# Performance work log

Hardware: AMD Instinct MI355X
Metric: run time of the kernel (lower is better)

Reference implementation:

```python
import jax, jax.numpy as jnp
import numpy as np

B, N, D = 64, 784, 768
H, HD, G = 32, 24, 2
HID = 3072
SCALE = HD ** -0.5
EPS = 1e-6


def _ln(x, g, b):
    m = jnp.mean(x, -1, keepdims=True)
    v = jnp.mean((x - m) ** 2, -1, keepdims=True)
    return (x - m) * jax.lax.rsqrt(v + EPS) * g + b


def setup_inputs() -> dict:
    key = jax.random.key(0)
    ks = jax.random.split(key, 12)
    def rn(k, shape, s=0.02):
        return (jax.random.normal(k, shape) * s).astype(jnp.float32)
    return {
        'x_cls': jax.random.normal(ks[0], (B, 1, D), jnp.float32),
        'x_img': jax.random.normal(ks[1], (B, N, D), jnp.float32),
        'ln1_g': jnp.ones((D,), jnp.float32), 'ln1_b': jnp.zeros((D,), jnp.float32),
        'Wq': rn(ks[2], (D, D)), 'bq': jnp.zeros((D,), jnp.float32),
        'Wk': rn(ks[3], (D, D)), 'bk': jnp.zeros((D,), jnp.float32),
        'Wv': rn(ks[4], (D, D)), 'bv': jnp.zeros((D,), jnp.float32),
        'w1_W': rn(ks[5], (H, H), 0.1), 'w1_b': jnp.zeros((H,), jnp.float32),
        'w2_W': rn(ks[6], (H, H), 0.1), 'w2_b': jnp.zeros((H,), jnp.float32),
        'proj_W': rn(ks[7], (D, D)), 'proj_b': jnp.zeros((D,), jnp.float32),
        'ln2_g': jnp.ones((D,), jnp.float32), 'ln2_b': jnp.zeros((D,), jnp.float32),
        'fc1_W': rn(ks[8], (G, HID // G, D // G)), 'fc1_b': jnp.zeros((G, HID // G), jnp.float32),
        'fc2_W': rn(ks[9], (G, D // G, HID // G)), 'fc2_b': jnp.zeros((G, D // G), jnp.float32),
    }


def reference(x_cls, x_img, ln1_g, ln1_b, Wq, bq, Wk, bk, Wv, bv,
              w1_W, w1_b, w2_W, w2_b, proj_W, proj_b, ln2_g, ln2_b,
              fc1_W, fc1_b, fc2_W, fc2_b):
    # --- ClassAttention (non-mismatch path), dropout = identity (eval) ---
    u = jnp.concatenate([x_cls, x_img], axis=1)  # [B, M, D], M = N+1
    M = u.shape[1]
    n = _ln(u, ln1_g, ln1_b)
    q = ((n[:, :1] @ Wq + bq).reshape(B, 1, H, HD).transpose(0, 2, 1, 3)) * SCALE  # [B,H,1,HD]
    k = (n @ Wk + bk).reshape(B, M, H, HD).transpose(0, 2, 1, 3)                   # [B,H,M,HD]
    v = (n @ Wv + bv).reshape(B, M, H, HD).transpose(0, 2, 1, 3)
    attn = jnp.einsum('bhqd,bhkd->bhqk', q, k)  # [B,H,1,M]
    # interactive score mixing across heads (w1 pre-softmax, w2 post-softmax)
    attn = attn + jnp.einsum('bhqk,hg->bgqk', attn, w1_W) + w1_b[None, :, None, None]
    attn = jax.nn.softmax(attn, axis=-1)
    attn = attn + jnp.einsum('bhqk,hg->bgqk', attn, w2_W) + w2_b[None, :, None, None]
    o = jnp.einsum('bhqk,bhkd->bhqd', attn, v).transpose(0, 2, 1, 3).reshape(B, 1, D)
    x_cls = x_cls + (o @ proj_W + proj_b)
    # --- GroupConvMlp on the cls token (grouped 1x1 convs + channel shuffle) ---
    y = _ln(x_cls, ln2_g, ln2_b)
    h = jnp.einsum('btgc,goc->btgo', y.reshape(B, 1, G, D // G), fc1_W) + fc1_b  # group-major out channels
    h = jax.nn.gelu(h.reshape(B, 1, HID), approximate=False)
    # channel_shuffle(group=G): out channel b*gc+a = in channel a*G+b
    h = h.reshape(B, 1, HID // G, G).transpose(0, 1, 3, 2).reshape(B, 1, HID)
    z = jnp.einsum('btgc,goc->btgo', h.reshape(B, 1, G, HID // G), fc2_W) + fc2_b
    x_cls = x_cls + z.reshape(B, 1, D)
    return (x_cls, x_img)
```

## Files before the change

### kernel.cpp

```cpp
#include <hip/hip_runtime.h>
#include <hip/hip_bf16.h>
#include <math.h>

#define BB   64
#define NN   784
#define DD   768
#define HH   32
#define HD24 24
#define MM   785
#define HIDN 3072
#define QSCALE 0.20412414523193154f
#define LNEPS 1e-6f

#define WS_Q     0
#define WS_RS    49152
#define WS_RM    100352
#define WS_S1P   151552
#define WS_BQP   163840
#define WS_LMX   176128
#define WS_LSM   184320
#define WS_A2P   192512
#define WS_WMP   200704
#define WS_PS    208896
#define WS_C1    210432
#define WS_H2    259584
#define WS_O     456192
#define WS_E     505344
#define WS_T     2143744
#define WS_ZP    0

typedef __attribute__((ext_vector_type(8))) short bf16x8;
typedef __attribute__((ext_vector_type(4))) float f32x4;

__device__ __forceinline__ unsigned packbf(float a, float b) {
  union { __hip_bfloat162 h2; unsigned u; } cv;
  cv.h2 = __float22bfloat162_rn(make_float2(a, b));
  return cv.u;
}

__global__ __launch_bounds__(256) void k_q(
    const float* __restrict__ x_cls,
    const float* __restrict__ g1, const float* __restrict__ b1,
    const float* __restrict__ Wq, const float* __restrict__ bq,
    float* __restrict__ ws)
{
  const int b = blockIdx.y;
  const int oc0 = blockIdx.x * 64;
  const int t = threadIdx.x;
  const int lane = t & 63, wid = t >> 6;

  __shared__ __align__(16) float nc_l[DD];
  __shared__ float red4[4][64];
  __shared__ float rS[4], rQ[4];
  __shared__ float musd[2];

  float xv[3];
  float s = 0.f, q2 = 0.f;
#pragma unroll
  for (int k = 0; k < 3; ++k) {
    float v = x_cls[(size_t)b * DD + t + 256 * k];
    xv[k] = v; s += v; q2 += v * v;
  }
#pragma unroll
  for (int off = 1; off < 64; off <<= 1) { s += __shfl_xor(s, off); q2 += __shfl_xor(q2, off); }
  if (lane == 0) { rS[wid] = s; rQ[wid] = q2; }
  __syncthreads();
  if (t == 0) {
    float ss = rS[0] + rS[1] + rS[2] + rS[3];
    float qq = rQ[0] + rQ[1] + rQ[2] + rQ[3];
    float mu = ss * (1.f / DD);
    musd[0] = mu; musd[1] = rsqrtf(qq * (1.f / DD) - mu * mu + LNEPS);
  }
  __syncthreads();
  {
    float mu = musd[0], rs = musd[1];
#pragma unroll
    for (int k = 0; k < 3; ++k) {
      int d = t + 256 * k;
      nc_l[d] = (xv[k] - mu) * rs * g1[d] + b1[d];
    }
  }
  __syncthreads();

  const int oc = t & 63, ks = t >> 6;
  const float* wp = Wq + (size_t)(ks * 192) * DD + oc0 + oc;
  const float* ncp = nc_l + ks * 192;
  float a0 = 0.f, a1 = 0.f, a2 = 0.f, a3 = 0.f;
#pragma unroll 4
  for (int d = 0; d < 192; d += 4) {
    a0 += ncp[d + 0] * wp[(size_t)(d + 0) * DD];
    a1 += ncp[d + 1] * wp[(size_t)(d + 1) * DD];
    a2 += ncp[d + 2] * wp[(size_t)(d + 2) * DD];
    a3 += ncp[d + 3] * wp[(size_t)(d + 3) * DD];
  }
  red4[ks][oc] = (a0 + a1) + (a2 + a3);
  __syncthreads();
  if (t < 64) {
    int ocg = oc0 + t;
    ws[WS_Q + (size_t)b * DD + ocg] =
        (red4[0][t] + red4[1][t] + red4[2][t] + red4[3][t] + bq[ocg]) * QSCALE;
  }
}

__global__ __launch_bounds__(256) void k_gqk(
    const float* __restrict__ g1, const float* __restrict__ b1,
    const float* __restrict__ Wk, const float* __restrict__ w1W,
    float* __restrict__ ws)
{
  const int b = blockIdx.y;
  const int d0 = blockIdx.x * 128;
  const int t = threadIdx.x;

  __shared__ __align__(16) float q_l[DD];
  __shared__ float T1[HH * HH];
  __shared__ float qk_l[128][33];
  __shared__ float pS[8][HH], pB[8][HH];

  for (int i = t; i < DD; i += 256) q_l[i] = ws[WS_Q + (size_t)b * DD + i];
  for (int i = t; i < HH * HH; i += 256) {
    int g = i >> 5, h = i & 31;
    T1[i] = w1W[i] + ((g == h) ? 1.f : 0.f);
  }
  __syncthreads();

  {
    const int dl = t >> 1, gh = t & 1;
    const float4* wr = (const float4*)(Wk + (size_t)(d0 + dl) * DD + gh * 384);
    const float4* qr = (const float4*)(q_l + gh * 384);
#pragma unroll 4
    for (int gg = 0; gg < 16; ++gg) {
      float a = 0.f;
#pragma unroll
      for (int c = 0; c < 6; ++c) {
        float4 w = wr[gg * 6 + c];
        float4 p = qr[gg * 6 + c];
        a += w.x * p.x + w.y * p.y + w.z * p.z + w.w * p.w;
      }
      qk_l[dl][gh * 16 + gg] = a;
    }
  }
  __syncthreads();
  {
    const int h = t & 31, dg = t >> 5;
    float fb[16];
    float s1a = 0.f, bqa = 0.f;
#pragma unroll 2
    for (int dd = 0; dd < 16; ++dd) {
      int dl = dg * 16 + dd;
      float f = 0.f;
#pragma unroll 8
      for (int g = 0; g < HH; ++g) f += qk_l[dl][g] * T1[g * HH + h];
      float gq = g1[d0 + dl] * f;
      fb[dd] = gq;
      s1a += gq;
      bqa += b1[d0 + dl] * qk_l[dl][h];
    }
    const int kstep = (d0 >> 5) + (dg >> 1);
    const int nt = h >> 4;
    const int lane0 = (h & 15) + 32 * (dg & 1);
    uint4* GQB = (uint4*)(ws + WS_E) + (size_t)b * (24 * 2 * 64);
    GQB[(kstep * 2 + nt) * 64 + lane0] =
        make_uint4(packbf(fb[0], fb[1]), packbf(fb[2], fb[3]),
                   packbf(fb[4], fb[5]), packbf(fb[6], fb[7]));
    GQB[(kstep * 2 + nt) * 64 + lane0 + 16] =
        make_uint4(packbf(fb[8], fb[9]), packbf(fb[10], fb[11]),
                   packbf(fb[12], fb[13]), packbf(fb[14], fb[15]));
    pS[dg][h] = s1a; pB[dg][h] = bqa;
  }
  __syncthreads();
  if (t < HH) {
    float s = 0.f, bq = 0.f;
#pragma unroll
    for (int k = 0; k < 8; ++k) { s += pS[k][t]; bq += pB[k][t]; }
    ws[WS_S1P + ((size_t)b * 6 + blockIdx.x) * HH + t] = s;
    ws[WS_BQP + ((size_t)b * 6 + blockIdx.x) * HH + t] = bq;
  }
}

__global__ __launch_bounds__(256) void k_main1(
    const float* __restrict__ x_cls, const float* __restrict__ x_img,
    float* __restrict__ ws)
{
  const int b = blockIdx.y;
  const int m0 = blockIdx.x * 64;
  const int t = threadIdx.x;
  const int w = t >> 6;
  const int l = t & 63;
  const int lg = l >> 4;
  const int lm = l & 15;

  const uint4* GQ = (const uint4*)(ws + WS_E) + (size_t)b * (24 * 2 * 64);

  const int arow = m0 + w * 16 + lm;
  const bool av = (arow < MM);
  const int arc = av ? arow : 0;
  const float* asrc = (arc == 0) ? (x_cls + (size_t)b * DD)
                                 : (x_img + ((size_t)b * NN + (arc - 1)) * DD);

  f32x4 acc0 = {0.f, 0.f, 0.f, 0.f};
  f32x4 acc1 = {0.f, 0.f, 0.f, 0.f};
  float sl = 0.f, sq = 0.f;

#pragma unroll 4
  for (int kst = 0; kst < 24; ++kst) {
    float4 a0 = make_float4(0.f, 0.f, 0.f, 0.f);
    float4 a1 = make_float4(0.f, 0.f, 0.f, 0.f);
    if (av) {
      a0 = *(const float4*)(asrc + kst * 32 + 8 * lg);
      a1 = *(const float4*)(asrc + kst * 32 + 8 * lg + 4);
    }
    sl += (a0.x + a0.y) + (a0.z + a0.w) + (a1.x + a1.y) + (a1.z + a1.w);
    sq += a0.x*a0.x + a0.y*a0.y + a0.z*a0.z + a0.w*a0.w
        + a1.x*a1.x + a1.y*a1.y + a1.z*a1.z + a1.w*a1.w;
    union { uint4 u; bf16x8 h; } ua, ub0, ub1;
    ua.u = make_uint4(packbf(a0.x, a0.y), packbf(a0.z, a0.w),
                      packbf(a1.x, a1.y), packbf(a1.z, a1.w));
    ub0.u = GQ[(kst * 2 + 0) * 64 + l];
    ub1.u = GQ[(kst * 2 + 1) * 64 + l];
    acc0 = __builtin_amdgcn_mfma_f32_16x16x32_bf16(ua.h, ub0.h, acc0, 0, 0, 0);
    acc1 = __builtin_amdgcn_mfma_f32_16x16x32_bf16(ua.h, ub1.h, acc1, 0, 0, 0);
  }

  sl += __shfl_xor(sl, 16); sl += __shfl_xor(sl, 32);
  sq += __shfl_xor(sq, 16); sq += __shfl_xor(sq, 32);
  if (lg == 0 && av) {
    float mu = sl * (1.f / DD);
    float rs = rsqrtf(sq * (1.f / DD) - mu * mu + LNEPS);
    ws[WS_RS + (size_t)b * 800 + arow] = rs;
    ws[WS_RM + (size_t)b * 800 + arow] = rs * mu;
  }

  float* tb = ws + WS_T + (size_t)b * MM * HH;
#pragma unroll
  for (int r = 0; r < 4; ++r) {
    int row = m0 + w * 16 + 4 * lg + r;
    if (row < MM) {
      tb[(size_t)row * HH + lm] = acc0[r];
      tb[(size_t)row * HH + 16 + lm] = acc1[r];
    }
  }
}

__global__ __launch_bounds__(256) void k_sm_a(
    const float* __restrict__ bk,
    const float* __restrict__ w1W, const float* __restrict__ w1b,
    float* __restrict__ ws)
{
  const int cx = blockIdx.x, b = blockIdx.y;
  const int t = threadIdx.x;
  const int lane = t & 63, wid = t >> 6;

  __shared__ float T1[HH * HH];
  __shared__ float s1_sh[HH], c0_sh[HH], bq_sh[HH];
  __shared__ float red[4][HH];
  __shared__ float lmax_sh[HH];

  for (int i = t; i < HH * HH; i += 256) {
    int g = i >> 5, h = i & 31;
    T1[i] = w1W[i] + ((g == h) ? 1.f : 0.f);
  }
  if (t < HH) {
    float s1v = 0.f, bqv = 0.f;
#pragma unroll
    for (int p = 0; p < 6; ++p) {
      s1v += ws[WS_S1P + ((size_t)b * 6 + p) * HH + t];
      bqv += ws[WS_BQP + ((size_t)b * 6 + p) * HH + t];
    }
    const float* qp = ws + WS_Q + (size_t)b * DD + t * HD24;
#pragma unroll
    for (int j = 0; j < HD24; ++j) bqv += bk[t * HD24 + j] * qp[j];
    s1_sh[t] = s1v; bq_sh[t] = bqv;
  }
  __syncthreads();
  if (t < HH) {
    float c0 = w1b[t];
#pragma unroll
    for (int g = 0; g < HH; ++g) c0 += T1[g * HH + t] * bq_sh[g];
    c0_sh[t] = c0;
  }
  __syncthreads();

  const int m = cx * 256 + t;
  const bool vm = (m < MM);
  float a1[HH];
  if (vm) {
    const float* tb = ws + WS_T + ((size_t)b * MM + m) * HH;
    float rs = ws[WS_RS + (size_t)b * 800 + m];
    float rm = ws[WS_RM + (size_t)b * 800 + m];
#pragma unroll
    for (int q = 0; q < 8; ++q) {
      float4 tv = *(const float4*)(tb + q * 4);
      a1[4*q+0] = rs * tv.x - rm * s1_sh[4*q+0] + c0_sh[4*q+0];
      a1[4*q+1] = rs * tv.y - rm * s1_sh[4*q+1] + c0_sh[4*q+1];
      a1[4*q+2] = rs * tv.z - rm * s1_sh[4*q+2] + c0_sh[4*q+2];
      a1[4*q+3] = rs * tv.w - rm * s1_sh[4*q+3] + c0_sh[4*q+3];
    }
  } else {
#pragma unroll
    for (int h = 0; h < HH; ++h) a1[h] = -3.0e38f;
  }
#pragma unroll
  for (int h = 0; h < HH; ++h) {
    float v = a1[h];
#pragma unroll
    for (int off = 1; off < 64; off <<= 1) v = fmaxf(v, __shfl_xor(v, off));
    if (lane == 0) red[wid][h] = v;
  }
  __syncthreads();
  if (t < HH) {
    float v = fmaxf(fmaxf(red[0][t], red[1][t]), fmaxf(red[2][t], red[3][t]));
    lmax_sh[t] = v;
    ws[WS_LMX + ((size_t)b * 4 + cx) * HH + t] = v;
  }
  __syncthreads();
  float* E = ws + WS_E + (size_t)b * (HH * 800);
  if (vm) {
#pragma unroll
    for (int h = 0; h < HH; ++h) {
      float e = __expf(a1[h] - lmax_sh[h]);
      a1[h] = e;
      E[(size_t)h * 800 + m] = e;
    }
  } else {
#pragma unroll
    for (int h = 0; h < HH; ++h) a1[h] = 0.f;
  }
#pragma unroll
  for (int h = 0; h < HH; ++h) {
    float v = a1[h];
#pragma unroll
    for (int off = 1; off < 64; off <<= 1) v += __shfl_xor(v, off);
    if (lane == 0) red[wid][h] = v;
  }
  __syncthreads();
  if (t < HH)
    ws[WS_LSM + ((size_t)b * 4 + cx) * HH + t] = red[0][t] + red[1][t] + red[2][t] + red[3][t];
}

__global__ __launch_bounds__(256) void k_sm_b(
    const float* __restrict__ w2W, const float* __restrict__ w2b,
    float* __restrict__ ws)
{
  const int cx = blockIdx.x, b = blockIdx.y;
  const int t = threadIdx.x;
  const int lane = t & 63, wid = t >> 6;

  __shared__ __align__(16) float T2s[HH * HH];
  __shared__ float inv_sh[HH], w2b_sh[HH];
  __shared__ float red[4][HH];

  if (t < HH) {
    float l0 = ws[WS_LMX + ((size_t)b * 4 + 0) * HH + t];
    float l1 = ws[WS_LMX + ((size_t)b * 4 + 1) * HH + t];
    float l2 = ws[WS_LMX + ((size_t)b * 4 + 2) * HH + t];
    float l3 = ws[WS_LMX + ((size_t)b * 4 + 3) * HH + t];
    float gmax = fmaxf(fmaxf(l0, l1), fmaxf(l2, l3));
    float s = ws[WS_LSM + ((size_t)b * 4 + 0) * HH + t] * __expf(l0 - gmax)
            + ws[WS_LSM + ((size_t)b * 4 + 1) * HH + t] * __expf(l1 - gmax)
            + ws[WS_LSM + ((size_t)b * 4 + 2) * HH + t] * __expf(l2 - gmax)
            + ws[WS_LSM + ((size_t)b * 4 + 3) * HH + t] * __expf(l3 - gmax);
    float lcx = (cx == 0) ? l0 : (cx == 1) ? l1 : (cx == 2) ? l2 : l3;
    inv_sh[t] = __expf(lcx - gmax) / s;
    w2b_sh[t] = w2b[t];
  }
  __syncthreads();
  for (int i = t; i < HH * HH; i += 256) {
    int g = i >> 5, h = i & 31;
    T2s[i] = (w2W[i] + ((g == h) ? 1.f : 0.f)) * inv_sh[g];
  }
  __syncthreads();

  const int m = cx * 256 + t;
  float* E = ws + WS_E + (size_t)b * (HH * 800);
  float4 av[8];
#pragma unroll
  for (int q = 0; q < 8; ++q) av[q] = make_float4(0.f,0.f,0.f,0.f);
  float rm = 0.f;
  if (m < MM) {
    float rs = ws[WS_RS + (size_t)b * 800 + m];
    rm = ws[WS_RM + (size_t)b * 800 + m];
#pragma unroll 4
    for (int g = 0; g < HH; ++g) {
      float eg = E[(size_t)g * 800 + m];
#pragma unroll
      for (int q = 0; q < 8; ++q) {
        float4 t2 = *(const float4*)&T2s[g * HH + q * 4];
        av[q].x += eg * t2.x; av[q].y += eg * t2.y;
        av[q].z += eg * t2.z; av[q].w += eg * t2.w;
      }
    }
#pragma unroll
    for (int q = 0; q < 8; ++q) {
      av[q].x += w2b_sh[q*4+0]; av[q].y += w2b_sh[q*4+1];
      av[q].z += w2b_sh[q*4+2]; av[q].w += w2b_sh[q*4+3];
      E[(size_t)(q*4+0) * 800 + m] = av[q].x * rs;
      E[(size_t)(q*4+1) * 800 + m] = av[q].y * rs;
      E[(size_t)(q*4+2) * 800 + m] = av[q].z * rs;
      E[(size_t)(q*4+3) * 800 + m] = av[q].w * rs;
    }
  } else if (m < 800) {
#pragma unroll
    for (int h = 0; h < HH; ++h) E[(size_t)h * 800 + m] = 0.f;
  }
#pragma unroll
  for (int h = 0; h < HH; ++h) {
    float v = ((const float*)&av[h >> 2])[h & 3];
#pragma unroll
    for (int off = 1; off < 64; off <<= 1) v += __shfl_xor(v, off);
    if (lane == 0) red[wid][h] = v;
  }
  __syncthreads();
  if (t < HH)
    ws[WS_A2P + ((size_t)b * 4 + cx) * HH + t] = red[0][t] + red[1][t] + red[2][t] + red[3][t];
  __syncthreads();
#pragma unroll
  for (int h = 0; h < HH; ++h) {
    float v = ((const float*)&av[h >> 2])[h & 3] * rm;
#pragma unroll
    for (int off = 1; off < 64; off <<= 1) v += __shfl_xor(v, off);
    if (lane == 0) red[wid][h] = v;
  }
  __syncthreads();
  if (t < HH)
    ws[WS_WMP + ((size_t)b * 4 + cx) * HH + t] = red[0][t] + red[1][t] + red[2][t] + red[3][t];
}

__global__ __launch_bounds__(256) void k_wsum(
    const float* __restrict__ x_cls, const float* __restrict__ x_img,
    float* __restrict__ out, float* __restrict__ ws)
{
  const int b = blockIdx.y;
  const int d0 = blockIdx.x * 64;
  const int t = threadIdx.x;
  const int dseg = t & 15;
  const int msub = (t >> 4) & 3;
  const int hb = (t >> 6) * 8;
  const int wv = t >> 6;

  __shared__ __align__(16) float w_s[HH][36];
  const float* W = ws + WS_E + (size_t)b * (HH * 800);
  float* out_img = out + (size_t)BB * DD;

  float acc[8][4];
#pragma unroll
  for (int j = 0; j < 8; ++j)
#pragma unroll
    for (int c = 0; c < 4; ++c) acc[j][c] = 0.f;

  float4 pu[8], pun[8];
  float4 pwn;

  auto LOADU = [&](int mc, float4* dst) {
#pragma unroll
    for (int i = 0; i < 8; ++i) {
      int m = mc * 32 + msub * 8 + i;
      if (m < MM) {
        const float* src = (m == 0) ? (x_cls + (size_t)b * DD)
                                    : (x_img + ((size_t)b * NN + (m - 1)) * DD);
        dst[i] = *(const float4*)(src + d0 + dseg * 4);
      } else dst[i] = make_float4(0.f,0.f,0.f,0.f);
    }
  };

  LOADU(0, pu);
  {
    float4 pw = *(const float4*)(W + (size_t)(t >> 3) * 800 + (t & 7) * 4);
    *(float4*)&w_s[t >> 3][(t & 7) * 4] = pw;
  }
  __syncthreads();

  for (int mc = 0; mc < 25; ++mc) {
    if (mc < 24) {
      pwn = *(const float4*)(W + (size_t)(t >> 3) * 800 + (mc + 1) * 32 + (t & 7) * 4);
      LOADU(mc + 1, pun);
    }
#pragma unroll
    for (int j = 0; j < 8; ++j) {
      float4 wA = *(const float4*)&w_s[hb + j][msub * 8];
      float4 wB = *(const float4*)&w_s[hb + j][msub * 8 + 4];
      float wv0 = wA.x, wv1 = wA.y, wv2 = wA.z, wv3 = wA.w;
      float wv4 = wB.x, wv5 = wB.y, wv6 = wB.z, wv7 = wB.w;
      acc[j][0] += wv0*pu[0].x + wv1*pu[1].x + wv2*pu[2].x + wv3*pu[3].x
                 + wv4*pu[4].x + wv5*pu[5].x + wv6*pu[6].x + wv7*pu[7].x;
      acc[j][1] += wv0*pu[0].y + wv1*pu[1].y + wv2*pu[2].y + wv3*pu[3].y
                 + wv4*pu[4].y + wv5*pu[5].y + wv6*pu[6].y + wv7*pu[7].y;
      acc[j][2] += wv0*pu[0].z + wv1*pu[1].z + wv2*pu[2].z + wv3*pu[3].z
                 + wv4*pu[4].z + wv5*pu[5].z + wv6*pu[6].z + wv7*pu[7].z;
      acc[j][3] += wv0*pu[0].w + wv1*pu[1].w + wv2*pu[2].w + wv3*pu[3].w
                 + wv4*pu[4].w + wv5*pu[5].w + wv6*pu[6].w + wv7*pu[7].w;
    }
#pragma unroll
    for (int i = 0; i < 8; ++i) {
      if ((i >> 1) == wv) {
        int m = mc * 32 + msub * 8 + i;
        if (m >= 1 && m < MM)
          *(float4*)(out_img + ((size_t)b * NN + (m - 1)) * DD + d0 + dseg * 4) = pu[i];
      }
    }
    __syncthreads();
    if (mc < 24) {
      *(float4*)&w_s[t >> 3][(t & 7) * 4] = pwn;
#pragma unroll
      for (int i = 0; i < 8; ++i) pu[i] = pun[i];
    }
    __syncthreads();
  }

#pragma unroll
  for (int j = 0; j < 8; ++j)
#pragma unroll
    for (int c = 0; c < 4; ++c) {
      float v = acc[j][c];
      v += __shfl_xor(v, 16);
      v += __shfl_xor(v, 32);
      acc[j][c] = v;
    }
  if (msub == 0) {
    float* R = ws + WS_T + (size_t)b * HH * DD;
#pragma unroll
    for (int j = 0; j < 8; ++j)
      *(float4*)(R + (size_t)(hb + j) * DD + d0 + dseg * 4) =
          make_float4(acc[j][0], acc[j][1], acc[j][2], acc[j][3]);
  }
}

__global__ __launch_bounds__(192) void k_att_o(
    const float* __restrict__ g1, const float* __restrict__ b1,
    const float* __restrict__ Wv, const float* __restrict__ bv,
    float* __restrict__ ws)
{
  const int h = blockIdx.x;
  const int b = blockIdx.y;
  const int t = threadIdx.x;

  __shared__ __align__(16) float agg_l[DD];
  __shared__ float red[8][25];
  __shared__ float a2wm[2];

  if (t == 0) {
    float a = 0.f;
#pragma unroll
    for (int c = 0; c < 4; ++c) a += ws[WS_A2P + ((size_t)b * 4 + c) * HH + h];
    a2wm[0] = a;
  }
  if (t == 1) {
    float w = 0.f;
#pragma unroll
    for (int c = 0; c < 4; ++c) w += ws[WS_WMP + ((size_t)b * 4 + c) * HH + h];
    a2wm[1] = w;
  }
  __syncthreads();
  const float A2 = a2wm[0], WM = a2wm[1];
  const float* R = ws + WS_T + ((size_t)b * HH + h) * DD;
  for (int i = t; i < DD; i += 192)
    agg_l[i] = g1[i] * (R[i] - WM) + b1[i] * A2;
  __syncthreads();

  const int oc = t % 24, ks = t / 24;
  const float* wv = Wv + (size_t)(ks * 96) * DD + h * HD24 + oc;
  const float* ag = agg_l + ks * 96;
  float a0 = 0.f, a1 = 0.f, a2 = 0.f, a3 = 0.f;
#pragma unroll 4
  for (int d = 0; d < 96; d += 4) {
    a0 += ag[d + 0] * wv[(size_t)(d + 0) * DD];
    a1 += ag[d + 1] * wv[(size_t)(d + 1) * DD];
    a2 += ag[d + 2] * wv[(size_t)(d + 2) * DD];
    a3 += ag[d + 3] * wv[(size_t)(d + 3) * DD];
  }
  red[ks][oc] = (a0 + a1) + (a2 + a3);
  __syncthreads();
  if (t < 24) {
    float o = A2 * bv[h * HD24 + t];
#pragma unroll
    for (int k = 0; k < 8; ++k) o += red[k][t];
    ws[WS_O + (size_t)b * DD + h * HD24 + t] = o;
  }
}

__global__ __launch_bounds__(256) void k_proj2(
    const float* __restrict__ x_cls,
    const float* __restrict__ projW, const float* __restrict__ projb,
    float* __restrict__ ws)
{
  const int b = blockIdx.y;
  const int oc0 = blockIdx.x * 64;
  const int t = threadIdx.x;

  __shared__ __align__(16) float o_l[DD];
  __shared__ float red4[4][64];

  for (int i = t; i < DD; i += 256) o_l[i] = ws[WS_O + (size_t)b * DD + i];
  __syncthreads();

  const int oc = t & 63, ks = t >> 6;
  const float* wp = projW + (size_t)(ks * 192) * DD + oc0 + oc;
  const float* op = o_l + ks * 192;
  float a0 = 0.f, a1 = 0.f, a2 = 0.f, a3 = 0.f;
#pragma unroll 4
  for (int d = 0; d < 192; d += 4) {
    a0 += op[d + 0] * wp[(size_t)(d + 0) * DD];
    a1 += op[d + 1] * wp[(size_t)(d + 1) * DD];
    a2 += op[d + 2] * wp[(size_t)(d + 2) * DD];
    a3 += op[d + 3] * wp[(size_t)(d + 3) * DD];
  }
  red4[ks][oc] = (a0 + a1) + (a2 + a3);
  __syncthreads();
  if (t < 64) {
    int ocg = oc0 + t;
    float c1 = red4[0][t] + red4[1][t] + red4[2][t] + red4[3][t]
             + projb[ocg] + x_cls[(size_t)b * DD + ocg];
    ws[WS_C1 + (size_t)b * DD + ocg] = c1;
    float cs = c1, cq = c1 * c1;
#pragma unroll
    for (int off = 1; off < 64; off <<= 1) { cs += __shfl_xor(cs, off); cq += __shfl_xor(cq, off); }
    if (t == 0) {
      ws[WS_PS + ((size_t)b * 12 + blockIdx.x) * 2 + 0] = cs;
      ws[WS_PS + ((size_t)b * 12 + blockIdx.x) * 2 + 1] = cq;
    }
  }
}

__global__ __launch_bounds__(256) void k_fc1(
    const float* __restrict__ fc1W, const float* __restrict__ fc1b,
    const float* __restrict__ g2, const float* __restrict__ b2,
    float* __restrict__ ws)
{
  const int g = blockIdx.x / 48;
  const int oc0 = (blockIdx.x % 48) * 32;
  const int t = threadIdx.x;
  const int txo = t & 7, tyb = t >> 3;

  __shared__ float y_s[64][65];
  __shared__ float w_s[32][65];
  __shared__ float mv[64][2];

  if (t < 64) {
    float s = 0.f, q = 0.f;
#pragma unroll
    for (int p = 0; p < 12; ++p) {
      s += ws[WS_PS + ((size_t)t * 12 + p) * 2 + 0];
      q += ws[WS_PS + ((size_t)t * 12 + p) * 2 + 1];
    }
    float mu = s * (1.f / DD);
    mv[t][0] = mu;
    mv[t][1] = rsqrtf(q * (1.f / DD) - mu * mu + LNEPS);
  }
  __syncthreads();

  float acc[2][4];
#pragma unroll
  for (int i = 0; i < 2; ++i)
#pragma unroll
    for (int j = 0; j < 4; ++j) acc[i][j] = 0.f;

#pragma unroll 1
  for (int kc = 0; kc < 6; ++kc) {
    {
      int r = t >> 2;
      float mu = mv[r][0], rs = mv[r][1];
#pragma unroll
      for (int p = 0; p < 4; ++p) {
        int c = (t & 3) * 4 + p * 16;
        int gc = g * 384 + kc * 64 + c;
        float4 v = *(const float4*)(ws + WS_C1 + (size_t)r * DD + gc);
        float4 gg = *(const float4*)(g2 + gc);
        float4 bb = *(const float4*)(b2 + gc);
        y_s[r][c+0] = (v.x - mu) * rs * gg.x + bb.x;
        y_s[r][c+1] = (v.y - mu) * rs * gg.y + bb.y;
        y_s[r][c+2] = (v.z - mu) * rs * gg.z + bb.z;
        y_s[r][c+3] = (v.w - mu) * rs * gg.w + bb.w;
      }
      int rw = t >> 3;
#pragma unroll
      for (int p = 0; p < 2; ++p) {
        int c = (t & 7) * 4 + p * 32;
        float4 w = *(const float4*)(fc1W + ((size_t)(g * 1536 + oc0 + rw)) * 384 + kc * 64 + c);
        w_s[rw][c+0] = w.x; w_s[rw][c+1] = w.y; w_s[rw][c+2] = w.z; w_s[rw][c+3] = w.w;
      }
    }
    __syncthreads();
#pragma unroll 4
    for (int kk = 0; kk < 64; ++kk) {
      float y0 = y_s[2*tyb+0][kk], y1 = y_s[2*tyb+1][kk];
      float w0 = w_s[4*txo+0][kk], w1 = w_s[4*txo+1][kk];
      float w2 = w_s[4*txo+2][kk], w3 = w_s[4*txo+3][kk];
      acc[0][0] += y0*w0; acc[0][1] += y0*w1; acc[0][2] += y0*w2; acc[0][3] += y0*w3;
      acc[1][0] += y1*w0; acc[1][1] += y1*w1; acc[1][2] += y1*w2; acc[1][3] += y1*w3;
    }
    __syncthreads();
  }

  float* H2 = ws + WS_H2;
#pragma unroll
  for (int i = 0; i < 2; ++i) {
    int bb = 2 * tyb + i;
#pragma unroll
    for (int j = 0; j < 4; ++j) {
      int oc = oc0 + 4 * txo + j;
      float v = acc[i][j] + fc1b[g * 1536 + oc];
      v = 0.5f * v * (1.f + erff(v * 0.70710678118654752f));
      H2[(size_t)bb * HIDN + (oc & 1) * 1536 + g * 768 + (oc >> 1)] = v;
    }
  }
}

__global__ __launch_bounds__(256) void k_fc2(
    const float* __restrict__ fc2W, float* __restrict__ ws)
{
  const int oc0 = blockIdx.x * 32;
  const int kq = blockIdx.y;
  const int g = blockIdx.z;
  const int t = threadIdx.x;
  const int txo = t & 7, tyb = t >> 3;

  __shared__ float h_s[64][65];
  __shared__ float w_s[32][65];

  float acc[2][4];
#pragma unroll
  for (int i = 0; i < 2; ++i)
#pragma unroll
    for (int j = 0; j < 4; ++j) acc[i][j] = 0.f;

  const float* H2 = ws + WS_H2;

#pragma unroll 1
  for (int kc = 0; kc < 6; ++kc) {
    {
      int r = t >> 2;
#pragma unroll
      for (int p = 0; p < 4; ++p) {
        int c = (t & 3) * 4 + p * 16;
        float4 v = *(const float4*)(H2 + (size_t)r * HIDN + g * 1536 + kq * 384 + kc * 64 + c);
        h_s[r][c+0] = v.x; h_s[r][c+1] = v.y; h_s[r][c+2] = v.z; h_s[r][c+3] = v.w;
      }
      int rw = t >> 3;
#pragma unroll
      for (int p = 0; p < 2; ++p) {
        int c = (t & 7) * 4 + p * 32;
        float4 w = *(const float4*)(fc2W + ((size_t)(g * 384 + oc0 + rw)) * 1536 + kq * 384 + kc * 64 + c);
        w_s[rw][c+0] = w.x; w_s[rw][c+1] = w.y; w_s[rw][c+2] = w.z; w_s[rw][c+3] = w.w;
      }
    }
    __syncthreads();
#pragma unroll 4
    for (int kk = 0; kk < 64; ++kk) {
      float y0 = h_s[2*tyb+0][kk], y1 = h_s[2*tyb+1][kk];
      float w0 = w_s[4*txo+0][kk], w1 = w_s[4*txo+1][kk];
      float w2 = w_s[4*txo+2][kk], w3 = w_s[4*txo+3][kk];
      acc[0][0] += y0*w0; acc[0][1] += y0*w1; acc[0][2] += y0*w2; acc[0][3] += y0*w3;
      acc[1][0] += y1*w0; acc[1][1] += y1*w1; acc[1][2] += y1*w2; acc[1][3] += y1*w3;
    }
    __syncthreads();
  }

  float* ZP = ws + WS_ZP + (size_t)kq * BB * DD;
#pragma unroll
  for (int i = 0; i < 2; ++i)
#pragma unroll
    for (int j = 0; j < 4; ++j)
      ZP[(size_t)(2 * tyb + i) * DD + g * 384 + oc0 + 4 * txo + j] = acc[i][j];
}

__global__ __launch_bounds__(256) void k_final(
    const float* __restrict__ fc2b, float* __restrict__ out, const float* __restrict__ ws)
{
  int idx = blockIdx.x * 256 + threadIdx.x;
  int d = idx % DD;
  float v = ws[WS_C1 + idx] + fc2b[d];
#pragma unroll
  for (int kq = 0; kq < 4; ++kq) v += ws[WS_ZP + (size_t)kq * BB * DD + idx];
  out[idx] = v;
}

extern "C" void kernel_launch(void* const* d_in, const int* in_sizes, int n_in,
                              void* d_out, int out_size, void* d_ws, size_t ws_size,
                              hipStream_t stream)
{
  (void)in_sizes; (void)n_in; (void)out_size; (void)ws_size;
  const float* x_cls = (const float*)d_in[0];
  const float* x_img = (const float*)d_in[1];
  const float* ln1_g = (const float*)d_in[2];
  const float* ln1_b = (const float*)d_in[3];
  const float* Wq    = (const float*)d_in[4];
  const float* bq    = (const float*)d_in[5];
  const float* Wk    = (const float*)d_in[6];
  const float* bk    = (const float*)d_in[7];
  const float* Wv    = (const float*)d_in[8];
  const float* bv    = (const float*)d_in[9];
  const float* w1W   = (const float*)d_in[10];
  const float* w1b   = (const float*)d_in[11];
  const float* w2W   = (const float*)d_in[12];
  const float* w2b   = (const float*)d_in[13];
  const float* projW = (const float*)d_in[14];
  const float* projb = (const float*)d_in[15];
  const float* ln2_g = (const float*)d_in[16];
  const float* ln2_b = (const float*)d_in[17];
  const float* fc1W  = (const float*)d_in[18];
  const float* fc1b  = (const float*)d_in[19];
  const float* fc2W  = (const float*)d_in[20];
  const float* fc2b  = (const float*)d_in[21];
  float* out = (float*)d_out;
  float* ws  = (float*)d_ws;

  k_q    <<<dim3(12, 64), dim3(256), 0, stream>>>(x_cls, ln1_g, ln1_b, Wq, bq, ws);
  k_gqk  <<<dim3(6, 64),  dim3(256), 0, stream>>>(ln1_g, ln1_b, Wk, w1W, ws);
  k_main1<<<dim3(13, 64), dim3(256), 0, stream>>>(x_cls, x_img, ws);
  k_sm_a <<<dim3(4, 64),  dim3(256), 0, stream>>>(bk, w1W, w1b, ws);
  k_sm_b <<<dim3(4, 64),  dim3(256), 0, stream>>>(w2W, w2b, ws);
  k_wsum <<<dim3(12, 64), dim3(256), 0, stream>>>(x_cls, x_img, out, ws);
  k_att_o<<<dim3(32, 64), dim3(192), 0, stream>>>(ln1_g, ln1_b, Wv, bv, ws);
  k_proj2<<<dim3(12, 64), dim3(256), 0, stream>>>(x_cls, projW, projb, ws);
  k_fc1  <<<dim3(96),     dim3(256), 0, stream>>>(fc1W, fc1b, ln2_g, ln2_b, ws);
  k_fc2  <<<dim3(12, 4, 2), dim3(256), 0, stream>>>(fc2W, ws);
  k_final<<<dim3(192),    dim3(256), 0, stream>>>(fc2b, out, ws);
}
```

Baseline: 316.3 us.

## Split k_wsum token loop across two half-blocks and reduce partials via shared memory

Result: faster. 304.0 us (-3.9%).

```diff
diff --git a/kernel.cpp b/kernel.cpp
--- a/kernel.cpp
+++ b/kernel.cpp
@@ -425,22 +425,32 @@
     ws[WS_WMP + ((size_t)b * 4 + cx) * HH + t] = red[0][t] + red[1][t] + red[2][t] + red[3][t];
 }
 
-__global__ __launch_bounds__(256) void k_wsum(
+__global__ __launch_bounds__(512) void k_wsum(
     const float* __restrict__ x_cls, const float* __restrict__ x_img,
     float* __restrict__ out, float* __restrict__ ws)
 {
   const int b = blockIdx.y;
   const int d0 = blockIdx.x * 64;
   const int t = threadIdx.x;
+  const int wv = t >> 6;
+  const int mh = wv >> 2;
+  const int hw = wv & 3;
+  const int hb = hw * 8;
   const int dseg = t & 15;
   const int msub = (t >> 4) & 3;
-  const int hb = (t >> 6) * 8;
-  const int wv = t >> 6;
-
-  __shared__ __align__(16) float w_s[HH][36];
+  const int mcBeg = mh * 13;
+  const int mcN = 13 - mh;
+
+  __shared__ __align__(16) float w_s[2][HH][36];
+  __shared__ __align__(16) float r_s[HH][68];
+
   const float* W = ws + WS_E + (size_t)b * (HH * 800);
   float* out_img = out + (size_t)BB * DD;
 
+  const int sh = t >> 8;
+  const int si = t & 255;
+  const int shN = 13 - sh;
+
   float acc[8][4];
 #pragma unroll
   for (int j = 0; j < 8; ++j)
@@ -450,11 +460,11 @@
   float4 pu[8], pun[8];
   float4 pwn;
 
-  auto LOADU = [&](int mc, float4* dst) {
+  auto LOADU = [&](int j, float4* dst) {
 #pragma unroll
     for (int i = 0; i < 8; ++i) {
-      int m = mc * 32 + msub * 8 + i;
-      if (m < MM) {
+      int m = (mcBeg + j) * 32 + msub * 8 + i;
+      if (j < mcN && m < MM) {
         const float* src = (m == 0) ? (x_cls + (size_t)b * DD)
                                     : (x_img + ((size_t)b * NN + (m - 1)) * DD);
         dst[i] = *(const float4*)(src + d0 + dseg * 4);
@@ -464,42 +474,46 @@
 
   LOADU(0, pu);
   {
-    float4 pw = *(const float4*)(W + (size_t)(t >> 3) * 800 + (t & 7) * 4);
-    *(float4*)&w_s[t >> 3][(t & 7) * 4] = pw;
-  }
-  __syncthreads();
-
-  for (int mc = 0; mc < 25; ++mc) {
-    if (mc < 24) {
-      pwn = *(const float4*)(W + (size_t)(t >> 3) * 800 + (mc + 1) * 32 + (t & 7) * 4);
-      LOADU(mc + 1, pun);
-    }
-#pragma unroll
-    for (int j = 0; j < 8; ++j) {
-      float4 wA = *(const float4*)&w_s[hb + j][msub * 8];
-      float4 wB = *(const float4*)&w_s[hb + j][msub * 8 + 4];
-      float wv0 = wA.x, wv1 = wA.y, wv2 = wA.z, wv3 = wA.w;
-      float wv4 = wB.x, wv5 = wB.y, wv6 = wB.z, wv7 = wB.w;
-      acc[j][0] += wv0*pu[0].x + wv1*pu[1].x + wv2*pu[2].x + wv3*pu[3].x
-                 + wv4*pu[4].x + wv5*pu[5].x + wv6*pu[6].x + wv7*pu[7].x;
-      acc[j][1] += wv0*pu[0].y + wv1*pu[1].y + wv2*pu[2].y + wv3*pu[3].y
-                 + wv4*pu[4].y + wv5*pu[5].y + wv6*pu[6].y + wv7*pu[7].y;
-      acc[j][2] += wv0*pu[0].z + wv1*pu[1].z + wv2*pu[2].z + wv3*pu[3].z
-                 + wv4*pu[4].z + wv5*pu[5].z + wv6*pu[6].z + wv7*pu[7].z;
-      acc[j][3] += wv0*pu[0].w + wv1*pu[1].w + wv2*pu[2].w + wv3*pu[3].w
-                 + wv4*pu[4].w + wv5*pu[5].w + wv6*pu[6].w + wv7*pu[7].w;
-    }
-#pragma unroll
-    for (int i = 0; i < 8; ++i) {
-      if ((i >> 1) == wv) {
-        int m = mc * 32 + msub * 8 + i;
-        if (m >= 1 && m < MM)
-          *(float4*)(out_img + ((size_t)b * NN + (m - 1)) * DD + d0 + dseg * 4) = pu[i];
+    float4 pw = *(const float4*)(W + (size_t)(si >> 3) * 800 + (sh * 13) * 32 + (si & 7) * 4);
+    *(float4*)&w_s[sh][si >> 3][(si & 7) * 4] = pw;
+  }
+  __syncthreads();
+
+  for (int j = 0; j < 13; ++j) {
+    if (j + 1 < 13) {
+      if (j + 1 < shN)
+        pwn = *(const float4*)(W + (size_t)(si >> 3) * 800 + (sh * 13 + j + 1) * 32 + (si & 7) * 4);
+      LOADU(j + 1, pun);
+    }
+    if (j < mcN) {
+#pragma unroll
+      for (int jj = 0; jj < 8; ++jj) {
+        float4 wA = *(const float4*)&w_s[mh][hb + jj][msub * 8];
+        float4 wB = *(const float4*)&w_s[mh][hb + jj][msub * 8 + 4];
+        float wv0 = wA.x, wv1 = wA.y, wv2 = wA.z, wv3 = wA.w;
+        float wv4 = wB.x, wv5 = wB.y, wv6 = wB.z, wv7 = wB.w;
+        acc[jj][0] += wv0*pu[0].x + wv1*pu[1].x + wv2*pu[2].x + wv3*pu[3].x
+                    + wv4*pu[4].x + wv5*pu[5].x + wv6*pu[6].x + wv7*pu[7].x;
+        acc[jj][1] += wv0*pu[0].y + wv1*pu[1].y + wv2*pu[2].y + wv3*pu[3].y
+                    + wv4*pu[4].y + wv5*pu[5].y + wv6*pu[6].y + wv7*pu[7].y;
+        acc[jj][2] += wv0*pu[0].z + wv1*pu[1].z + wv2*pu[2].z + wv3*pu[3].z
+                    + wv4*pu[4].z + wv5*pu[5].z + wv6*pu[6].z + wv7*pu[7].z;
+        acc[jj][3] += wv0*pu[0].w + wv1*pu[1].w + wv2*pu[2].w + wv3*pu[3].w
+                    + wv4*pu[4].w + wv5*pu[5].w + wv6*pu[6].w + wv7*pu[7].w;
       }
+#pragma unroll
+      for (int i = 0; i < 8; ++i) {
+        if ((i >> 1) == hw) {
+          int m = (mcBeg + j) * 32 + msub * 8 + i;
+          if (m >= 1 && m < MM)
+            *(float4*)(out_img + ((size_t)b * NN + (m - 1)) * DD + d0 + dseg * 4) = pu[i];
+        }
+      }
     }
     __syncthreads();
-    if (mc < 24) {
-      *(float4*)&w_s[t >> 3][(t & 7) * 4] = pwn;
+    if (j + 1 < 13) {
+      if (j + 1 < shN)
+        *(float4*)&w_s[sh][si >> 3][(si & 7) * 4] = pwn;
 #pragma unroll
       for (int i = 0; i < 8; ++i) pu[i] = pun[i];
     }
@@ -515,12 +529,22 @@
       v += __shfl_xor(v, 32);
       acc[j][c] = v;
     }
-  if (msub == 0) {
+  if (mh == 1 && msub == 0) {
+#pragma unroll
+    for (int j = 0; j < 8; ++j)
+      *(float4*)&r_s[hb + j][dseg * 4] =
+          make_float4(acc[j][0], acc[j][1], acc[j][2], acc[j][3]);
+  }
+  __syncthreads();
+  if (mh == 0 && msub == 0) {
     float* R = ws + WS_T + (size_t)b * HH * DD;
 #pragma unroll
-    for (int j = 0; j < 8; ++j)
+    for (int j = 0; j < 8; ++j) {
+      float4 rv = *(const float4*)&r_s[hb + j][dseg * 4];
       *(float4*)(R + (size_t)(hb + j) * DD + d0 + dseg * 4) =
-          make_float4(acc[j][0], acc[j][1], acc[j][2], acc[j][3]);
+          make_float4(acc[j][0] + rv.x, acc[j][1] + rv.y,
+                      acc[j][2] + rv.z, acc[j][3] + rv.w);
+    }
   }
 }
 
@@ -808,7 +832,7 @@
   k_main1<<<dim3(13, 64), dim3(256), 0, stream>>>(x_cls, x_img, ws);
   k_sm_a <<<dim3(4, 64),  dim3(256), 0, stream>>>(bk, w1W, w1b, ws);
   k_sm_b <<<dim3(4, 64),  dim3(256), 0, stream>>>(w2W, w2b, ws);
-  k_wsum <<<dim3(12, 64), dim3(256), 0, stream>>>(x_cls, x_img, out, ws);
+  k_wsum <<<dim3(12, 64), dim3(512), 0, stream>>>(x_cls, x_img, out, ws);
   k_att_o<<<dim3(32, 64), dim3(192), 0, stream>>>(ln1_g, ln1_b, Wv, bv, ws);
   k_proj2<<<dim3(12, 64), dim3(256), 0, stream>>>(x_cls, projW, projb, ws);
   k_fc1  <<<dim3(96),     dim3(256), 0, stream>>>(fc1W, fc1b, ln2_g, ln2_b, ws);
```
